# Kernel optimization log

Hardware: AMD Instinct MI355X
Metric: run time of the kernel (lower is better)

## Reference

```python
import jax, jax.numpy as jnp
import numpy as np

S, P = 64, 32          # scenes, pedestrians per scene (uniform)
N = S * P              # total pedestrians = 2048
H, E = 64, 64          # h_dim, embedding_dim
D1, D2 = 512, 1024     # mlp_pre_pool hidden, bottleneck_dim
EPS = 1e-5             # torch BatchNorm1d eps


def _batchnorm(x, gamma, beta):
    # Training-mode BN with per-scene batch stats (matches the per-scene
    # loop in the original, where BN sees one scene's num_ped^2 rows).
    # x: [S, P*P, D]
    mu = jnp.mean(x, axis=1, keepdims=True)
    var = jnp.mean(jnp.square(x - mu), axis=1, keepdims=True)  # biased var, as torch BN
    return (x - mu) * jax.lax.rsqrt(var + EPS) * gamma + beta


def setup_inputs() -> dict:
    key = jax.random.key(0)
    ks = jax.random.split(key, 16)
    h_states = jax.random.normal(ks[0], (1, N, H), jnp.float32)
    starts = jnp.arange(S, dtype=jnp.int32) * P
    seq_start_end = jnp.stack([starts, starts + P], axis=1)  # [S, 2]
    end_pos = jax.random.normal(ks[1], (N, 2), jnp.float32)
    rel_pos = jax.random.normal(ks[2], (N, 2), jnp.float32)  # unused (pooling_dim=2) but a fwd arg
    sc = 0.05
    params = dict(
        W_embed=jax.random.normal(ks[3], (2, E), jnp.float32) * sc,
        b_embed=jnp.zeros((E,), jnp.float32),
        W1=jax.random.normal(ks[4], (E + H, D1), jnp.float32) * sc,
        b1=jnp.zeros((D1,), jnp.float32),
        g1=jnp.ones((D1,), jnp.float32),
        be1=jnp.zeros((D1,), jnp.float32),
        W2=jax.random.normal(ks[5], (D1, D2), jnp.float32) * sc,
        b2=jnp.zeros((D2,), jnp.float32),
        g2=jnp.ones((D2,), jnp.float32),
        be2=jnp.zeros((D2,), jnp.float32),
    )
    return dict(h_states=h_states, seq_start_end=seq_start_end,
                end_pos=end_pos, rel_pos=rel_pos, **params)


def reference(h_states, seq_start_end, end_pos, rel_pos,
              W_embed, b_embed, W1, b1, g1, be1, W2, b2, g2, be2):
    # Uniform scenes: seq_start_end delimits S contiguous blocks of P peds.
    pos = end_pos.reshape(S, P, 2)
    h = h_states.reshape(N, H).reshape(S, P, H)
    # Original indexing: row (k*P + j) -> pos[j] - pos[k], hidden[j];
    # the final view(P, P, -1).max(1) maxes over j for each k.
    rel = pos[:, None, :, :] - pos[:, :, None, :]          # [S, Pk, Pj, 2]
    emb = rel @ W_embed + b_embed                          # [S, Pk, Pj, E]
    hid = jnp.broadcast_to(h[:, None, :, :], (S, P, P, H)) # hidden of j
    x = jnp.concatenate([emb, hid], axis=-1).reshape(S, P * P, E + H)
    x = jax.nn.relu(_batchnorm(x @ W1 + b1, g1, be1))      # [S, P*P, 512]
    x = jax.nn.relu(_batchnorm(x @ W2 + b2, g2, be2))      # [S, P*P, 1024]
    pool_h = x.reshape(S, P, P, D2).max(axis=2)            # max over j
    return pool_h.reshape(N, D2)
```

## Files before the change

### kernel.cpp

```cpp
#include <hip/hip_runtime.h>
#include <hip/hip_bf16.h>

#define S_ 64
#define P_ 32
#define N_ 2048
#define H_ 64
#define E_ 64
#define D1_ 512
#define D2_ 1024
#define EPS_ 1e-5f

typedef unsigned short u16;
using bf16x8 = __attribute__((ext_vector_type(8))) __bf16;
using floatx4 = __attribute__((ext_vector_type(4))) float;

__device__ inline u16 f2bf(float x) {
    unsigned u = __float_as_uint(x);
    unsigned r = (u + 0x7fffu + ((u >> 16) & 1u)) >> 16;
    return (u16)r;
}
__device__ inline unsigned bf2pack(float lo, float hi) {
    return (unsigned)f2bf(lo) | ((unsigned)f2bf(hi) << 16);
}

__global__ __launch_bounds__(512)
void k_prep(const float* __restrict__ pos, const float* __restrict__ h,
            const float* __restrict__ We, const float* __restrict__ W1,
            const float* __restrict__ g1, const float* __restrict__ be1,
            const float* __restrict__ W2,
            float* __restrict__ A, float* __restrict__ Bv, u16* __restrict__ w2t) {
    __shared__ float smem[64 * 65];
    const int bid = blockIdx.x;
    const int tid = threadIdx.x;
    if (bid < S_) {
        const int s = bid;
        const int d = tid;
        float* hs = smem;
        float* ps = smem + 2048;
        for (int i = tid; i < P_ * H_; i += 512) hs[i] = h[(size_t)s * P_ * H_ + i];
        if (tid < 64) ps[tid] = pos[s * 64 + tid];
        __syncthreads();
        float wq0 = 0.f, wq1 = 0.f;
        for (int e = 0; e < E_; ++e) {
            float wv = W1[e * D1_ + d];
            wq0 += We[e] * wv;
            wq1 += We[E_ + e] * wv;
        }
        float w[P_];
#pragma unroll
        for (int j = 0; j < P_; ++j) w[j] = 0.f;
        const float4* h4 = (const float4*)hs;
        for (int e4 = 0; e4 < 16; ++e4) {
            const float c0 = W1[(E_ + e4 * 4 + 0) * D1_ + d];
            const float c1 = W1[(E_ + e4 * 4 + 1) * D1_ + d];
            const float c2 = W1[(E_ + e4 * 4 + 2) * D1_ + d];
            const float c3 = W1[(E_ + e4 * 4 + 3) * D1_ + d];
#pragma unroll
            for (int j = 0; j < P_; ++j) {
                float4 hv = h4[j * 16 + e4];
                w[j] += hv.x * c0 + hv.y * c1 + hv.z * c2 + hv.w * c3;
            }
        }
        float sw = 0.f, sww = 0.f, su = 0.f, suu = 0.f;
#pragma unroll
        for (int j = 0; j < P_; ++j) {
            float u = ps[2 * j] * wq0 + ps[2 * j + 1] * wq1;
            w[j] += u;
            sw += w[j]; sww += w[j] * w[j];
            su += u;    suu += u * u;
        }
        const float mw = sw * (1.f / P_), mu = su * (1.f / P_);
        const float var = (sww * (1.f / P_) - mw * mw) + (suu * (1.f / P_) - mu * mu);
        const float sc = rsqrtf(var + EPS_) * g1[d];
        const float bb = be1[d];
#pragma unroll
        for (int j = 0; j < P_; ++j) {
            float u = ps[2 * j] * wq0 + ps[2 * j + 1] * wq1;
            A[(size_t)(s * P_ + j) * D1_ + d] = (w[j] - mw) * sc + bb;
            Bv[(size_t)(s * P_ + j) * D1_ + d] = (u - mu) * sc;
        }
    } else {
        const int b2 = bid - S_;
        const int bi = b2 & 15;
        const int bj = b2 >> 4;
        const int tx = tid & 63, ty = tid >> 6;
        float (*tile)[65] = (float (*)[65])smem;
#pragma unroll
        for (int i = 0; i < 64; i += 8)
            tile[ty + i][tx] = W2[(size_t)(bj * 64 + ty + i) * D2_ + bi * 64 + tx];
        __syncthreads();
#pragma unroll
        for (int i = 0; i < 64; i += 8)
            w2t[(size_t)(bi * 64 + ty + i) * D1_ + bj * 64 + tx] = f2bf(tile[tx][ty + i]);
    }
}

__global__ __launch_bounds__(256, 2)
void k_gemm(const float* __restrict__ A, const float* __restrict__ B,
            const u16* __restrict__ w2t,
            float* __restrict__ maxv, float* __restrict__ minv,
            float* __restrict__ psum, float* __restrict__ psumsq) {
    __shared__ u16 As[128 * 64];
    __shared__ u16 Ws[256 * 64];
    const int cs = blockIdx.x;
    const int mt = blockIdx.y;
    const int s = mt >> 3, rb = mt & 7;
    const int pedb = rb << 2;
    const int N0 = cs << 8;
    const int tid = threadIdx.x;
    const int wave = tid >> 6, lane = tid & 63;
    const int wm = wave >> 1, wn = wave & 1;
    const int quad = lane >> 4, l16 = lane & 15;
    const int lrow = lane >> 3, lchk = lane & 7;
    const int gchk = lchk ^ lrow;

    const int sj = tid >> 3, sc8 = tid & 7;
    const float* Aj = A + ((size_t)(s * 32 + sj) << 9) + (sc8 << 3);
    const float* Bp = B + ((size_t)(s * 32 + pedb) << 9) + (sc8 << 3);
    const int swz = (sc8 ^ (sj & 7)) << 3;

    floatx4 acc[4][8] = {};

    for (int it = 0; it < 8; ++it) {
        const int k0 = it << 6;
#pragma unroll
        for (int t = 0; t < 8; ++t) {
            const int rbase = (wave << 6) + (t << 3);
            const u16* gb = w2t + (size_t)(N0 + rbase + lrow) * D1_ + (k0 + (gchk << 3));
            __builtin_amdgcn_global_load_lds(
                (const __attribute__((address_space(1))) void*)gb,
                (__attribute__((address_space(3))) void*)(Ws + (rbase << 6)), 16, 0, 0);
        }
#pragma unroll
        for (int p = 0; p < 4; ++p) {
            const int r = (p << 5) + sj;
            const float4 alo = *(const float4*)(Aj + k0);
            const float4 ahi = *(const float4*)(Aj + k0 + 4);
            const float4 blo = *(const float4*)(Bp + ((size_t)p << 9) + k0);
            const float4 bhi = *(const float4*)(Bp + ((size_t)p << 9) + k0 + 4);
            uint4 o;
            o.x = bf2pack(fmaxf(alo.x - blo.x, 0.f), fmaxf(alo.y - blo.y, 0.f));
            o.y = bf2pack(fmaxf(alo.z - blo.z, 0.f), fmaxf(alo.w - blo.w, 0.f));
            o.z = bf2pack(fmaxf(ahi.x - bhi.x, 0.f), fmaxf(ahi.y - bhi.y, 0.f));
            o.w = bf2pack(fmaxf(ahi.z - bhi.z, 0.f), fmaxf(ahi.w - bhi.w, 0.f));
            *(uint4*)(As + (r << 6) + swz) = o;
        }
        __syncthreads();
#pragma unroll
        for (int kk = 0; kk < 2; ++kk) {
            const int ck = (kk << 2) + quad;
            const int po = (ck ^ (l16 & 7)) << 3;
            bf16x8 af[4], wf[8];
#pragma unroll
            for (int tm = 0; tm < 4; ++tm) {
                const int row = (wm << 6) + (tm << 4) + l16;
                af[tm] = *(const bf16x8*)(As + (row << 6) + po);
            }
#pragma unroll
            for (int tn = 0; tn < 8; ++tn) {
                const int row = (wn << 7) + (tn << 4) + l16;
                wf[tn] = *(const bf16x8*)(Ws + (row << 6) + po);
            }
#pragma unroll
            for (int tm = 0; tm < 4; ++tm)
#pragma unroll
                for (int tn = 0; tn < 8; ++tn)
                    acc[tm][tn] = __builtin_amdgcn_mfma_f32_16x16x32_bf16(
                        af[tm], wf[tn], acc[tm][tn], 0, 0, 0);
        }
        __syncthreads();
    }

#pragma unroll
    for (int tn = 0; tn < 8; ++tn) {
        const int col = N0 + (wn << 7) + (tn << 4) + l16;
        float wsum = 0.f, wsq = 0.f;
#pragma unroll
        for (int gp = 0; gp < 2; ++gp) {
            float vmax = -3.4e38f, vmin = 3.4e38f, vs = 0.f, vq = 0.f;
#pragma unroll
            for (int tm = gp * 2; tm < gp * 2 + 2; ++tm)
#pragma unroll
                for (int r = 0; r < 4; ++r) {
                    float v = acc[tm][tn][r];
                    vmax = fmaxf(vmax, v);
                    vmin = fminf(vmin, v);
                    vs += v;
                    vq += v * v;
                }
#pragma unroll
            for (int off = 16; off < 64; off <<= 1) {
                vmax = fmaxf(vmax, __shfl_xor(vmax, off));
                vmin = fminf(vmin, __shfl_xor(vmin, off));
                vs += __shfl_xor(vs, off);
                vq += __shfl_xor(vq, off);
            }
            if (quad == 0) {
                const int kg = s * 32 + pedb + (wm << 1) + gp;
                maxv[(size_t)kg * D2_ + col] = vmax;
                minv[(size_t)kg * D2_ + col] = vmin;
            }
            wsum += vs;
            wsq += vq;
        }
        if (quad == 0) {
            const int slot = (s << 4) + (rb << 1) + wm;
            psum[(size_t)slot * D2_ + col] = wsum;
            psumsq[(size_t)slot * D2_ + col] = wsq;
        }
    }
}

__global__ void k_final(const float* __restrict__ maxv, const float* __restrict__ minv,
                        const float* __restrict__ psum, const float* __restrict__ psumsq,
                        const float* __restrict__ g2, const float* __restrict__ be2,
                        float* __restrict__ out) {
    const int c = blockIdx.x * 256 + threadIdx.x;
    const int s = blockIdx.y;
    float sm = 0.f, sq = 0.f;
#pragma unroll
    for (int t = 0; t < 16; ++t) {
        sm += psum[(size_t)(s * 16 + t) * D2_ + c];
        sq += psumsq[(size_t)(s * 16 + t) * D2_ + c];
    }
    const float mu = sm * (1.f / 1024.f);
    const float var = sq * (1.f / 1024.f) - mu * mu;
    const float inv = rsqrtf(var + EPS_);
    const float scale = g2[c] * inv;
    const float bb = be2[c];
    const float* src = (scale >= 0.f) ? maxv : minv;
    for (int k = 0; k < 32; ++k) {
        const float v = src[(size_t)(s * 32 + k) * D2_ + c];
        out[(size_t)(s * 32 + k) * D2_ + c] = fmaxf((v - mu) * scale + bb, 0.f);
    }
}

extern "C" void kernel_launch(void* const* d_in, const int* in_sizes, int n_in,
                              void* d_out, int out_size, void* d_ws, size_t ws_size,
                              hipStream_t stream) {
    const float* h_states = (const float*)d_in[0];
    const float* end_pos = (const float*)d_in[2];
    const float* W_embed = (const float*)d_in[4];
    const float* W1 = (const float*)d_in[6];
    const float* g1 = (const float*)d_in[8];
    const float* be1 = (const float*)d_in[9];
    const float* W2 = (const float*)d_in[10];
    const float* g2 = (const float*)d_in[12];
    const float* be2 = (const float*)d_in[13];
    float* out = (float*)d_out;

    float* Abuf = (float*)d_ws;
    float* Bbuf = Abuf + 1048576;
    float* maxv = Bbuf + 1048576;
    float* minv = maxv + 2097152;
    float* psum = minv + 2097152;
    float* psumsq = psum + 1048576;
    u16* w2t = (u16*)(psumsq + 1048576);

    k_prep<<<dim3(S_ + 128), dim3(512), 0, stream>>>(end_pos, h_states, W_embed, W1,
                                                     g1, be1, W2, Abuf, Bbuf, w2t);
    k_gemm<<<dim3(4, 512), dim3(256), 0, stream>>>(Abuf, Bbuf, w2t, maxv, minv, psum, psumsq);
    k_final<<<dim3(4, 64), dim3(256), 0, stream>>>(maxv, minv, psum, psumsq, g2, be2, out);
}
```

Before: 199.1 us.

## Split prep across d-quarters and widen GEMM tile to 512 columns with 8 waves

The prep kernel now uses 256 blocks instead of 64, each covering a quarter of the D1 dimension with four pedestrian groups. Per-column BN statistics are combined through a shared-memory reduction, which gives more parallelism and fewer registers per thread. The GEMM kernel moves to 512-thread blocks covering 512 output columns, so each A tile (built with relu(A-B) and bf16 conversion) is reused across twice as many columns and the grid is halved. The trade-off is a doubled W2 tile in LDS and the launch bound of 512 threads with 4 blocks, which may cause register or occupancy pressure.

```diff
diff --git a/kernel.cpp b/kernel.cpp
--- a/kernel.cpp
+++ b/kernel.cpp
@@ -29,26 +29,28 @@
             const float* __restrict__ g1, const float* __restrict__ be1,
             const float* __restrict__ W2,
             float* __restrict__ A, float* __restrict__ Bv, u16* __restrict__ w2t) {
-    __shared__ float smem[64 * 65];
+    __shared__ float smem[4160];
     const int bid = blockIdx.x;
     const int tid = threadIdx.x;
-    if (bid < S_) {
-        const int s = bid;
-        const int d = tid;
+    if (bid < 256) {
+        const int s = bid >> 2, dq = bid & 3;
+        const int jg = tid >> 7, dl = tid & 127;
+        const int d = (dq << 7) + dl;
         float* hs = smem;
         float* ps = smem + 2048;
+        float* red = smem + 2112;
         for (int i = tid; i < P_ * H_; i += 512) hs[i] = h[(size_t)s * P_ * H_ + i];
         if (tid < 64) ps[tid] = pos[s * 64 + tid];
         __syncthreads();
         float wq0 = 0.f, wq1 = 0.f;
         for (int e = 0; e < E_; ++e) {
-            float wv = W1[e * D1_ + d];
+            const float wv = W1[e * D1_ + d];
             wq0 += We[e] * wv;
             wq1 += We[E_ + e] * wv;
         }
-        float w[P_];
-#pragma unroll
-        for (int j = 0; j < P_; ++j) w[j] = 0.f;
+        float w[8], u[8];
+#pragma unroll
+        for (int jj = 0; jj < 8; ++jj) w[jj] = 0.f;
         const float4* h4 = (const float4*)hs;
         for (int e4 = 0; e4 < 16; ++e4) {
             const float c0 = W1[(E_ + e4 * 4 + 0) * D1_ + d];
@@ -56,31 +58,45 @@
             const float c2 = W1[(E_ + e4 * 4 + 2) * D1_ + d];
             const float c3 = W1[(E_ + e4 * 4 + 3) * D1_ + d];
 #pragma unroll
-            for (int j = 0; j < P_; ++j) {
-                float4 hv = h4[j * 16 + e4];
-                w[j] += hv.x * c0 + hv.y * c1 + hv.z * c2 + hv.w * c3;
+            for (int jj = 0; jj < 8; ++jj) {
+                const float4 hv = h4[((jg << 3) + jj) * 16 + e4];
+                w[jj] += hv.x * c0 + hv.y * c1 + hv.z * c2 + hv.w * c3;
             }
         }
         float sw = 0.f, sww = 0.f, su = 0.f, suu = 0.f;
 #pragma unroll
-        for (int j = 0; j < P_; ++j) {
-            float u = ps[2 * j] * wq0 + ps[2 * j + 1] * wq1;
-            w[j] += u;
-            sw += w[j]; sww += w[j] * w[j];
-            su += u;    suu += u * u;
-        }
-        const float mw = sw * (1.f / P_), mu = su * (1.f / P_);
-        const float var = (sww * (1.f / P_) - mw * mw) + (suu * (1.f / P_) - mu * mu);
+        for (int jj = 0; jj < 8; ++jj) {
+            const int j = (jg << 3) + jj;
+            u[jj] = ps[2 * j] * wq0 + ps[2 * j + 1] * wq1;
+            w[jj] += u[jj];
+            sw += w[jj]; sww += w[jj] * w[jj];
+            su += u[jj]; suu += u[jj] * u[jj];
+        }
+        red[(jg << 7) + dl] = sw;
+        red[512 + (jg << 7) + dl] = sww;
+        red[1024 + (jg << 7) + dl] = su;
+        red[1536 + (jg << 7) + dl] = suu;
+        __syncthreads();
+        float tw = 0.f, tww = 0.f, tu = 0.f, tuu = 0.f;
+#pragma unroll
+        for (int g = 0; g < 4; ++g) {
+            tw += red[(g << 7) + dl];
+            tww += red[512 + (g << 7) + dl];
+            tu += red[1024 + (g << 7) + dl];
+            tuu += red[1536 + (g << 7) + dl];
+        }
+        const float mw = tw * (1.f / P_), mu = tu * (1.f / P_);
+        const float var = (tww * (1.f / P_) - mw * mw) + (tuu * (1.f / P_) - mu * mu);
         const float sc = rsqrtf(var + EPS_) * g1[d];
         const float bb = be1[d];
 #pragma unroll
-        for (int j = 0; j < P_; ++j) {
-            float u = ps[2 * j] * wq0 + ps[2 * j + 1] * wq1;
-            A[(size_t)(s * P_ + j) * D1_ + d] = (w[j] - mw) * sc + bb;
-            Bv[(size_t)(s * P_ + j) * D1_ + d] = (u - mu) * sc;
+        for (int jj = 0; jj < 8; ++jj) {
+            const int j = (jg << 3) + jj;
+            A[(size_t)(s * P_ + j) * D1_ + d] = (w[jj] - mw) * sc + bb;
+            Bv[(size_t)(s * P_ + j) * D1_ + d] = (u[jj] - mu) * sc;
         }
     } else {
-        const int b2 = bid - S_;
+        const int b2 = bid - 256;
         const int bi = b2 & 15;
         const int bj = b2 >> 4;
         const int tx = tid & 63, ty = tid >> 6;
@@ -95,29 +111,24 @@
     }
 }
 
-__global__ __launch_bounds__(256, 2)
+__global__ __launch_bounds__(512, 4)
 void k_gemm(const float* __restrict__ A, const float* __restrict__ B,
             const u16* __restrict__ w2t,
             float* __restrict__ maxv, float* __restrict__ minv,
             float* __restrict__ psum, float* __restrict__ psumsq) {
     __shared__ u16 As[128 * 64];
-    __shared__ u16 Ws[256 * 64];
+    __shared__ u16 Ws[512 * 64];
     const int cs = blockIdx.x;
     const int mt = blockIdx.y;
     const int s = mt >> 3, rb = mt & 7;
     const int pedb = rb << 2;
-    const int N0 = cs << 8;
+    const int N0 = cs << 9;
     const int tid = threadIdx.x;
     const int wave = tid >> 6, lane = tid & 63;
-    const int wm = wave >> 1, wn = wave & 1;
+    const int wm = wave >> 2, wn = wave & 3;
     const int quad = lane >> 4, l16 = lane & 15;
     const int lrow = lane >> 3, lchk = lane & 7;
     const int gchk = lchk ^ lrow;
-
-    const int sj = tid >> 3, sc8 = tid & 7;
-    const float* Aj = A + ((size_t)(s * 32 + sj) << 9) + (sc8 << 3);
-    const float* Bp = B + ((size_t)(s * 32 + pedb) << 9) + (sc8 << 3);
-    const int swz = (sc8 ^ (sj & 7)) << 3;
 
     floatx4 acc[4][8] = {};
 
@@ -132,18 +143,22 @@
                 (__attribute__((address_space(3))) void*)(Ws + (rbase << 6)), 16, 0, 0);
         }
 #pragma unroll
-        for (int p = 0; p < 4; ++p) {
-            const int r = (p << 5) + sj;
-            const float4 alo = *(const float4*)(Aj + k0);
-            const float4 ahi = *(const float4*)(Aj + k0 + 4);
-            const float4 blo = *(const float4*)(Bp + ((size_t)p << 9) + k0);
-            const float4 bhi = *(const float4*)(Bp + ((size_t)p << 9) + k0 + 4);
+        for (int t = 0; t < 2; ++t) {
+            const int slot = tid + (t << 9);
+            const int r = slot >> 3, c = slot & 7;
+            const int j = r & 31, p = r >> 5;
+            const float* Aj = A + ((size_t)(s * 32 + j) << 9) + (c << 3) + k0;
+            const float* Bp = B + ((size_t)(s * 32 + pedb + p) << 9) + (c << 3) + k0;
+            const float4 alo = *(const float4*)Aj;
+            const float4 ahi = *(const float4*)(Aj + 4);
+            const float4 blo = *(const float4*)Bp;
+            const float4 bhi = *(const float4*)(Bp + 4);
             uint4 o;
             o.x = bf2pack(fmaxf(alo.x - blo.x, 0.f), fmaxf(alo.y - blo.y, 0.f));
             o.y = bf2pack(fmaxf(alo.z - blo.z, 0.f), fmaxf(alo.w - blo.w, 0.f));
             o.z = bf2pack(fmaxf(ahi.x - bhi.x, 0.f), fmaxf(ahi.y - bhi.y, 0.f));
             o.w = bf2pack(fmaxf(ahi.z - bhi.z, 0.f), fmaxf(ahi.w - bhi.w, 0.f));
-            *(uint4*)(As + (r << 6) + swz) = o;
+            *(uint4*)(As + (r << 6) + ((c ^ (r & 7)) << 3)) = o;
         }
         __syncthreads();
 #pragma unroll
@@ -182,7 +197,7 @@
             for (int tm = gp * 2; tm < gp * 2 + 2; ++tm)
 #pragma unroll
                 for (int r = 0; r < 4; ++r) {
-                    float v = acc[tm][tn][r];
+                    const float v = acc[tm][tn][r];
                     vmax = fmaxf(vmax, v);
                     vmin = fminf(vmin, v);
                     vs += v;
@@ -257,8 +272,8 @@
     float* psumsq = psum + 1048576;
     u16* w2t = (u16*)(psumsq + 1048576);
 
-    k_prep<<<dim3(S_ + 128), dim3(512), 0, stream>>>(end_pos, h_states, W_embed, W1,
-                                                     g1, be1, W2, Abuf, Bbuf, w2t);
-    k_gemm<<<dim3(4, 512), dim3(256), 0, stream>>>(Abuf, Bbuf, w2t, maxv, minv, psum, psumsq);
+    k_prep<<<dim3(384), dim3(512), 0, stream>>>(end_pos, h_states, W_embed, W1,
+                                                g1, be1, W2, Abuf, Bbuf, w2t);
+    k_gemm<<<dim3(2, 512), dim3(512), 0, stream>>>(Abuf, Bbuf, w2t, maxv, minv, psum, psumsq);
     k_final<<<dim3(4, 64), dim3(256), 0, stream>>>(maxv, minv, psum, psumsq, g2, be2, out);
 }
```

Result: slower. 684.6 us (+243.9%).

## Fuse prep, GEMM and finalize into one cooperative persistent kernel

Applied to the files above, without the earlier changes.

Merges the three launches into a single cooperative kernel that uses grid-wide syncs between the prep, GEMM and finalize phases. Each GEMM block now owns one M-tile and loops over all four column slices, where previously each block handled one (column slice, M-tile) pair. Prep is split into 256-thread units covering a quarter of the D1 columns, with a shared-memory reduction for the BN1 statistics. The aim is to remove launch gaps and kernel-boundary drains. The cost is fewer concurrent blocks and serialized column slices inside each block, which may reduce parallelism in the GEMM phase. A fallback path with three separate launches is kept.

```diff
diff --git a/kernel.cpp b/kernel.cpp
--- a/kernel.cpp
+++ b/kernel.cpp
@@ -1,5 +1,8 @@
 #include <hip/hip_runtime.h>
 #include <hip/hip_bf16.h>
+#include <hip/hip_cooperative_groups.h>
+
+namespace cg = cooperative_groups;
 
 #define S_ 64
 #define P_ 32
@@ -23,205 +26,208 @@
     return (unsigned)f2bf(lo) | ((unsigned)f2bf(hi) << 16);
 }
 
-__global__ __launch_bounds__(512)
-void k_prep(const float* __restrict__ pos, const float* __restrict__ h,
-            const float* __restrict__ We, const float* __restrict__ W1,
-            const float* __restrict__ g1, const float* __restrict__ be1,
-            const float* __restrict__ W2,
-            float* __restrict__ A, float* __restrict__ Bv, u16* __restrict__ w2t) {
-    __shared__ float smem[64 * 65];
-    const int bid = blockIdx.x;
-    const int tid = threadIdx.x;
-    if (bid < S_) {
-        const int s = bid;
-        const int d = tid;
-        float* hs = smem;
-        float* ps = smem + 2048;
-        for (int i = tid; i < P_ * H_; i += 512) hs[i] = h[(size_t)s * P_ * H_ + i];
-        if (tid < 64) ps[tid] = pos[s * 64 + tid];
-        __syncthreads();
-        float wq0 = 0.f, wq1 = 0.f;
-        for (int e = 0; e < E_; ++e) {
-            float wv = W1[e * D1_ + d];
-            wq0 += We[e] * wv;
-            wq1 += We[E_ + e] * wv;
+
+__device__ void prep_scene_256(int u, int tid, float* smem,
+                               const float* __restrict__ pos, const float* __restrict__ h,
+                               const float* __restrict__ We, const float* __restrict__ W1,
+                               const float* __restrict__ g1, const float* __restrict__ be1,
+                               float* __restrict__ A, float* __restrict__ Bv) {
+    const int s = u >> 2, dq = u & 3;
+    const int jg = tid >> 7, dl = tid & 127;
+    const int d = (dq << 7) + dl;
+    float* hs = smem;
+    float* ps = smem + 2048;
+    float* red = smem + 2112;
+    for (int i = tid; i < 2048; i += 256) hs[i] = h[(size_t)s * 2048 + i];
+    if (tid < 64) ps[tid] = pos[s * 64 + tid];
+    __syncthreads();
+    float wq0 = 0.f, wq1 = 0.f;
+    for (int e = 0; e < 64; ++e) {
+        const float wv = W1[e * 512 + d];
+        wq0 += We[e] * wv;
+        wq1 += We[64 + e] * wv;
+    }
+    float w[16], uu[16];
+#pragma unroll
+    for (int jj = 0; jj < 16; ++jj) w[jj] = 0.f;
+    const float4* h4 = (const float4*)hs;
+    for (int e4 = 0; e4 < 16; ++e4) {
+        const float c0 = W1[(64 + e4 * 4 + 0) * 512 + d];
+        const float c1 = W1[(64 + e4 * 4 + 1) * 512 + d];
+        const float c2 = W1[(64 + e4 * 4 + 2) * 512 + d];
+        const float c3 = W1[(64 + e4 * 4 + 3) * 512 + d];
+#pragma unroll
+        for (int jj = 0; jj < 16; ++jj) {
+            const float4 hv = h4[((jg << 4) + jj) * 16 + e4];
+            w[jj] += hv.x * c0 + hv.y * c1 + hv.z * c2 + hv.w * c3;
         }
-        float w[P_];
-#pragma unroll
-        for (int j = 0; j < P_; ++j) w[j] = 0.f;
-        const float4* h4 = (const float4*)hs;
-        for (int e4 = 0; e4 < 16; ++e4) {
-            const float c0 = W1[(E_ + e4 * 4 + 0) * D1_ + d];
-            const float c1 = W1[(E_ + e4 * 4 + 1) * D1_ + d];
-            const float c2 = W1[(E_ + e4 * 4 + 2) * D1_ + d];
-            const float c3 = W1[(E_ + e4 * 4 + 3) * D1_ + d];
-#pragma unroll
-            for (int j = 0; j < P_; ++j) {
-                float4 hv = h4[j * 16 + e4];
-                w[j] += hv.x * c0 + hv.y * c1 + hv.z * c2 + hv.w * c3;
-            }
-        }
-        float sw = 0.f, sww = 0.f, su = 0.f, suu = 0.f;
-#pragma unroll
-        for (int j = 0; j < P_; ++j) {
-            float u = ps[2 * j] * wq0 + ps[2 * j + 1] * wq1;
-            w[j] += u;
-            sw += w[j]; sww += w[j] * w[j];
-            su += u;    suu += u * u;
-        }
-        const float mw = sw * (1.f / P_), mu = su * (1.f / P_);
-        const float var = (sww * (1.f / P_) - mw * mw) + (suu * (1.f / P_) - mu * mu);
-        const float sc = rsqrtf(var + EPS_) * g1[d];
-        const float bb = be1[d];
-#pragma unroll
-        for (int j = 0; j < P_; ++j) {
-            float u = ps[2 * j] * wq0 + ps[2 * j + 1] * wq1;
-            A[(size_t)(s * P_ + j) * D1_ + d] = (w[j] - mw) * sc + bb;
-            Bv[(size_t)(s * P_ + j) * D1_ + d] = (u - mu) * sc;
-        }
-    } else {
-        const int b2 = bid - S_;
-        const int bi = b2 & 15;
-        const int bj = b2 >> 4;
-        const int tx = tid & 63, ty = tid >> 6;
-        float (*tile)[65] = (float (*)[65])smem;
-#pragma unroll
-        for (int i = 0; i < 64; i += 8)
-            tile[ty + i][tx] = W2[(size_t)(bj * 64 + ty + i) * D2_ + bi * 64 + tx];
-        __syncthreads();
-#pragma unroll
-        for (int i = 0; i < 64; i += 8)
-            w2t[(size_t)(bi * 64 + ty + i) * D1_ + bj * 64 + tx] = f2bf(tile[tx][ty + i]);
-    }
-}
-
-__global__ __launch_bounds__(256, 2)
-void k_gemm(const float* __restrict__ A, const float* __restrict__ B,
-            const u16* __restrict__ w2t,
-            float* __restrict__ maxv, float* __restrict__ minv,
-            float* __restrict__ psum, float* __restrict__ psumsq) {
-    __shared__ u16 As[128 * 64];
-    __shared__ u16 Ws[256 * 64];
-    const int cs = blockIdx.x;
-    const int mt = blockIdx.y;
-    const int s = mt >> 3, rb = mt & 7;
-    const int pedb = rb << 2;
-    const int N0 = cs << 8;
-    const int tid = threadIdx.x;
+    }
+    float sw = 0.f, sww = 0.f, su = 0.f, suu = 0.f;
+#pragma unroll
+    for (int jj = 0; jj < 16; ++jj) {
+        const int j = (jg << 4) + jj;
+        uu[jj] = ps[2 * j] * wq0 + ps[2 * j + 1] * wq1;
+        w[jj] += uu[jj];
+        sw += w[jj]; sww += w[jj] * w[jj];
+        su += uu[jj]; suu += uu[jj] * uu[jj];
+    }
+    red[(jg << 7) + dl] = sw;
+    red[256 + (jg << 7) + dl] = sww;
+    red[512 + (jg << 7) + dl] = su;
+    red[768 + (jg << 7) + dl] = suu;
+    __syncthreads();
+    const float tw = red[dl] + red[128 + dl];
+    const float tww = red[256 + dl] + red[384 + dl];
+    const float tu = red[512 + dl] + red[640 + dl];
+    const float tuu = red[768 + dl] + red[896 + dl];
+    const float mw = tw * (1.f / 32.f), mu2 = tu * (1.f / 32.f);
+    const float var = (tww * (1.f / 32.f) - mw * mw) + (tuu * (1.f / 32.f) - mu2 * mu2);
+    const float sc = rsqrtf(var + EPS_) * g1[d];
+    const float bb = be1[d];
+#pragma unroll
+    for (int jj = 0; jj < 16; ++jj) {
+        const int j = (jg << 4) + jj;
+        A[(size_t)(s * 32 + j) * 512 + d] = (w[jj] - mw) * sc + bb;
+        Bv[(size_t)(s * 32 + j) * 512 + d] = (uu[jj] - mu2) * sc;
+    }
+}
+
+__device__ void w2t_tile_256(int b2, int tid, void* smem,
+                             const float* __restrict__ W2, u16* __restrict__ w2t) {
+    float (*tile)[65] = (float (*)[65])smem;
+    const int bi = b2 & 15, bj = b2 >> 4;
+    const int tx = tid & 63, ty = tid >> 6;
+#pragma unroll
+    for (int i = 0; i < 64; i += 4)
+        tile[ty + i][tx] = W2[(size_t)(bj * 64 + ty + i) * 1024 + bi * 64 + tx];
+    __syncthreads();
+#pragma unroll
+    for (int i = 0; i < 64; i += 4)
+        w2t[(size_t)(bi * 64 + ty + i) * 512 + bj * 64 + tx] = f2bf(tile[tx][ty + i]);
+}
+
+__device__ void gemm_mtile(int mt, int tid, u16* As, u16* Ws,
+                           const float* __restrict__ A, const float* __restrict__ Bv,
+                           const u16* __restrict__ w2t,
+                           float* __restrict__ maxv, float* __restrict__ minv,
+                           float* __restrict__ psum, float* __restrict__ psumsq) {
     const int wave = tid >> 6, lane = tid & 63;
     const int wm = wave >> 1, wn = wave & 1;
     const int quad = lane >> 4, l16 = lane & 15;
     const int lrow = lane >> 3, lchk = lane & 7;
     const int gchk = lchk ^ lrow;
-
     const int sj = tid >> 3, sc8 = tid & 7;
-    const float* Aj = A + ((size_t)(s * 32 + sj) << 9) + (sc8 << 3);
-    const float* Bp = B + ((size_t)(s * 32 + pedb) << 9) + (sc8 << 3);
+    const int s2 = mt >> 3, rb = mt & 7;
+    const int pedb = rb << 2;
+    const float* Aj = A + ((size_t)(s2 * 32 + sj) << 9) + (sc8 << 3);
+    const float* Bp = Bv + ((size_t)(s2 * 32 + pedb) << 9) + (sc8 << 3);
     const int swz = (sc8 ^ (sj & 7)) << 3;
 
-    floatx4 acc[4][8] = {};
-
-    for (int it = 0; it < 8; ++it) {
-        const int k0 = it << 6;
-#pragma unroll
-        for (int t = 0; t < 8; ++t) {
-            const int rbase = (wave << 6) + (t << 3);
-            const u16* gb = w2t + (size_t)(N0 + rbase + lrow) * D1_ + (k0 + (gchk << 3));
-            __builtin_amdgcn_global_load_lds(
-                (const __attribute__((address_space(1))) void*)gb,
-                (__attribute__((address_space(3))) void*)(Ws + (rbase << 6)), 16, 0, 0);
+    for (int cs = 0; cs < 4; ++cs) {
+        const int N0 = cs << 8;
+        floatx4 acc[4][8] = {};
+        for (int it = 0; it < 8; ++it) {
+            const int k0 = it << 6;
+#pragma unroll
+            for (int t = 0; t < 8; ++t) {
+                const int rbase = (wave << 6) + (t << 3);
+                const u16* gb = w2t + (size_t)(N0 + rbase + lrow) * 512 + (k0 + (gchk << 3));
+                __builtin_amdgcn_global_load_lds(
+                    (const __attribute__((address_space(1))) void*)gb,
+                    (__attribute__((address_space(3))) void*)(Ws + (rbase << 6)), 16, 0, 0);
+            }
+#pragma unroll
+            for (int p = 0; p < 4; ++p) {
+                const int r = (p << 5) + sj;
+                const float4 alo = *(const float4*)(Aj + k0);
+                const float4 ahi = *(const float4*)(Aj + k0 + 4);
+                const float4 blo = *(const float4*)(Bp + ((size_t)p << 9) + k0);
+                const float4 bhi = *(const float4*)(Bp + ((size_t)p << 9) + k0 + 4);
+                uint4 o;
+                o.x = bf2pack(fmaxf(alo.x - blo.x, 0.f), fmaxf(alo.y - blo.y, 0.f));
+                o.y = bf2pack(fmaxf(alo.z - blo.z, 0.f), fmaxf(alo.w - blo.w, 0.f));
+                o.z = bf2pack(fmaxf(ahi.x - bhi.x, 0.f), fmaxf(ahi.y - bhi.y, 0.f));
+                o.w = bf2pack(fmaxf(ahi.z - bhi.z, 0.f), fmaxf(ahi.w - bhi.w, 0.f));
+                *(uint4*)(As + (r << 6) + swz) = o;
+            }
+            __syncthreads();
+#pragma unroll
+            for (int kk = 0; kk < 2; ++kk) {
+                const int ck = (kk << 2) + quad;
+                const int po = (ck ^ (l16 & 7)) << 3;
+                bf16x8 af[4], wf[8];
+#pragma unroll
+                for (int tm = 0; tm < 4; ++tm) {
+                    const int row = (wm << 6) + (tm << 4) + l16;
+                    af[tm] = *(const bf16x8*)(As + (row << 6) + po);
+                }
+#pragma unroll
+                for (int tn = 0; tn < 8; ++tn) {
+                    const int wrow = (wn << 7) + (tn << 4) + l16;
+                    wf[tn] = *(const bf16x8*)(Ws + (wrow << 6) + ((ck ^ (wrow & 7)) << 3));
+                }
+#pragma unroll
+                for (int tm = 0; tm < 4; ++tm)
+#pragma unroll
+                    for (int tn = 0; tn < 8; ++tn)
+                        acc[tm][tn] = __builtin_amdgcn_mfma_f32_16x16x32_bf16(
+                            af[tm], wf[tn], acc[tm][tn], 0, 0, 0);
+            }
+            __syncthreads();
         }
 #pragma unroll
-        for (int p = 0; p < 4; ++p) {
-            const int r = (p << 5) + sj;
-            const float4 alo = *(const float4*)(Aj + k0);
-            const float4 ahi = *(const float4*)(Aj + k0 + 4);
-            const float4 blo = *(const float4*)(Bp + ((size_t)p << 9) + k0);
-            const float4 bhi = *(const float4*)(Bp + ((size_t)p << 9) + k0 + 4);
-            uint4 o;
-            o.x = bf2pack(fmaxf(alo.x - blo.x, 0.f), fmaxf(alo.y - blo.y, 0.f));
-            o.y = bf2pack(fmaxf(alo.z - blo.z, 0.f), fmaxf(alo.w - blo.w, 0.f));
-            o.z = bf2pack(fmaxf(ahi.x - bhi.x, 0.f), fmaxf(ahi.y - bhi.y, 0.f));
-            o.w = bf2pack(fmaxf(ahi.z - bhi.z, 0.f), fmaxf(ahi.w - bhi.w, 0.f));
-            *(uint4*)(As + (r << 6) + swz) = o;
+        for (int tn = 0; tn < 8; ++tn) {
+            const int col = N0 + (wn << 7) + (tn << 4) + l16;
+            float wsum = 0.f, wsq = 0.f;
+#pragma unroll
+            for (int gp = 0; gp < 2; ++gp) {
+                float vmax = -3.4e38f, vmin = 3.4e38f, vs = 0.f, vq = 0.f;
+#pragma unroll
+                for (int tm = gp * 2; tm < gp * 2 + 2; ++tm)
+#pragma unroll
+                    for (int r = 0; r < 4; ++r) {
+                        const float v = acc[tm][tn][r];
+                        vmax = fmaxf(vmax, v);
+                        vmin = fminf(vmin, v);
+                        vs += v;
+                        vq += v * v;
+                    }
+#pragma unroll
+                for (int off = 16; off < 64; off <<= 1) {
+                    vmax = fmaxf(vmax, __shfl_xor(vmax, off));
+                    vmin = fminf(vmin, __shfl_xor(vmin, off));
+                    vs += __shfl_xor(vs, off);
+                    vq += __shfl_xor(vq, off);
+                }
+                if (quad == 0) {
+                    const int kg = s2 * 32 + pedb + (wm << 1) + gp;
+                    maxv[(size_t)kg * 1024 + col] = vmax;
+                    minv[(size_t)kg * 1024 + col] = vmin;
+                }
+                wsum += vs;
+                wsq += vq;
+            }
+            if (quad == 0) {
+                const int slot = (s2 << 4) + (rb << 1) + wm;
+                psum[(size_t)slot * 1024 + col] = wsum;
+                psumsq[(size_t)slot * 1024 + col] = wsq;
+            }
         }
-        __syncthreads();
-#pragma unroll
-        for (int kk = 0; kk < 2; ++kk) {
-            const int ck = (kk << 2) + quad;
-            const int po = (ck ^ (l16 & 7)) << 3;
-            bf16x8 af[4], wf[8];
-#pragma unroll
-            for (int tm = 0; tm < 4; ++tm) {
-                const int row = (wm << 6) + (tm << 4) + l16;
-                af[tm] = *(const bf16x8*)(As + (row << 6) + po);
-            }
-#pragma unroll
-            for (int tn = 0; tn < 8; ++tn) {
-                const int row = (wn << 7) + (tn << 4) + l16;
-                wf[tn] = *(const bf16x8*)(Ws + (row << 6) + po);
-            }
-#pragma unroll
-            for (int tm = 0; tm < 4; ++tm)
-#pragma unroll
-                for (int tn = 0; tn < 8; ++tn)
-                    acc[tm][tn] = __builtin_amdgcn_mfma_f32_16x16x32_bf16(
-                        af[tm], wf[tn], acc[tm][tn], 0, 0, 0);
-        }
-        __syncthreads();
-    }
-
-#pragma unroll
-    for (int tn = 0; tn < 8; ++tn) {
-        const int col = N0 + (wn << 7) + (tn << 4) + l16;
-        float wsum = 0.f, wsq = 0.f;
-#pragma unroll
-        for (int gp = 0; gp < 2; ++gp) {
-            float vmax = -3.4e38f, vmin = 3.4e38f, vs = 0.f, vq = 0.f;
-#pragma unroll
-            for (int tm = gp * 2; tm < gp * 2 + 2; ++tm)
-#pragma unroll
-                for (int r = 0; r < 4; ++r) {
-                    float v = acc[tm][tn][r];
-                    vmax = fmaxf(vmax, v);
-                    vmin = fminf(vmin, v);
-                    vs += v;
-                    vq += v * v;
-                }
-#pragma unroll
-            for (int off = 16; off < 64; off <<= 1) {
-                vmax = fmaxf(vmax, __shfl_xor(vmax, off));
-                vmin = fminf(vmin, __shfl_xor(vmin, off));
-                vs += __shfl_xor(vs, off);
-                vq += __shfl_xor(vq, off);
-            }
-            if (quad == 0) {
-                const int kg = s * 32 + pedb + (wm << 1) + gp;
-                maxv[(size_t)kg * D2_ + col] = vmax;
-                minv[(size_t)kg * D2_ + col] = vmin;
-            }
-            wsum += vs;
-            wsq += vq;
-        }
-        if (quad == 0) {
-            const int slot = (s << 4) + (rb << 1) + wm;
-            psum[(size_t)slot * D2_ + col] = wsum;
-            psumsq[(size_t)slot * D2_ + col] = wsq;
-        }
-    }
-}
-
-__global__ void k_final(const float* __restrict__ maxv, const float* __restrict__ minv,
-                        const float* __restrict__ psum, const float* __restrict__ psumsq,
-                        const float* __restrict__ g2, const float* __restrict__ be2,
-                        float* __restrict__ out) {
-    const int c = blockIdx.x * 256 + threadIdx.x;
-    const int s = blockIdx.y;
+    }
+}
+
+__device__ void final_unit_256(int u, int tid,
+                               const float* __restrict__ maxv, const float* __restrict__ minv,
+                               const float* __restrict__ psum, const float* __restrict__ psumsq,
+                               const float* __restrict__ g2, const float* __restrict__ be2,
+                               float* __restrict__ out) {
+    const int s3 = u >> 2;
+    const int c = ((u & 3) << 8) + tid;
     float sm = 0.f, sq = 0.f;
 #pragma unroll
     for (int t = 0; t < 16; ++t) {
-        sm += psum[(size_t)(s * 16 + t) * D2_ + c];
-        sq += psumsq[(size_t)(s * 16 + t) * D2_ + c];
+        sm += psum[(size_t)(s3 * 16 + t) * 1024 + c];
+        sq += psumsq[(size_t)(s3 * 16 + t) * 1024 + c];
     }
     const float mu = sm * (1.f / 1024.f);
     const float var = sq * (1.f / 1024.f) - mu * mu;
@@ -230,9 +236,79 @@
     const float bb = be2[c];
     const float* src = (scale >= 0.f) ? maxv : minv;
     for (int k = 0; k < 32; ++k) {
-        const float v = src[(size_t)(s * 32 + k) * D2_ + c];
-        out[(size_t)(s * 32 + k) * D2_ + c] = fmaxf((v - mu) * scale + bb, 0.f);
-    }
+        const float v = src[(size_t)(s3 * 32 + k) * 1024 + c];
+        out[(size_t)(s3 * 32 + k) * 1024 + c] = fmaxf((v - mu) * scale + bb, 0.f);
+    }
+}
+
+__global__ __launch_bounds__(256, 2)
+void k_all(const float* __restrict__ pos, const float* __restrict__ h,
+           const float* __restrict__ We, const float* __restrict__ W1,
+           const float* __restrict__ g1, const float* __restrict__ be1,
+           const float* __restrict__ W2, const float* __restrict__ g2,
+           const float* __restrict__ be2,
+           float* __restrict__ A, float* __restrict__ Bv, u16* __restrict__ w2t,
+           float* __restrict__ maxv, float* __restrict__ minv,
+           float* __restrict__ psum, float* __restrict__ psumsq,
+           float* __restrict__ out) {
+    __shared__ __align__(16) char smem_raw[49152];
+    cg::grid_group grid = cg::this_grid();
+    const int b = blockIdx.x;
+    const int g = gridDim.x;
+    const int tid = threadIdx.x;
+
+    for (int u = b; u < 384; u += g) {
+        if (u < 256)
+            prep_scene_256(u, tid, (float*)smem_raw, pos, h, We, W1, g1, be1, A, Bv);
+        else
+            w2t_tile_256(u - 256, tid, smem_raw, W2, w2t);
+        __syncthreads();
+    }
+    __threadfence();
+    grid.sync();
+
+    {
+        u16* As = (u16*)smem_raw;
+        u16* Ws = (u16*)(smem_raw + 16384);
+        for (int mt = b; mt < 512; mt += g)
+            gemm_mtile(mt, tid, As, Ws, A, Bv, w2t, maxv, minv, psum, psumsq);
+    }
+    __threadfence();
+    grid.sync();
+
+    for (int u = b; u < 256; u += g)
+        final_unit_256(u, tid, maxv, minv, psum, psumsq, g2, be2, out);
+}
+
+__global__ __launch_bounds__(256)
+void k_prep_fb(const float* __restrict__ pos, const float* __restrict__ h,
+               const float* __restrict__ We, const float* __restrict__ W1,
+               const float* __restrict__ g1, const float* __restrict__ be1,
+               const float* __restrict__ W2,
+               float* __restrict__ A, float* __restrict__ Bv, u16* __restrict__ w2t) {
+    __shared__ __align__(16) char smem_raw[16912];
+    const int bid = blockIdx.x;
+    if (bid < 256)
+        prep_scene_256(bid, threadIdx.x, (float*)smem_raw, pos, h, We, W1, g1, be1, A, Bv);
+    else
+        w2t_tile_256(bid - 256, threadIdx.x, smem_raw, W2, w2t);
+}
+
+__global__ __launch_bounds__(256, 2)
+void k_gemm_fb(const float* __restrict__ A, const float* __restrict__ Bv,
+               const u16* __restrict__ w2t,
+               float* __restrict__ maxv, float* __restrict__ minv,
+               float* __restrict__ psum, float* __restrict__ psumsq) {
+    __shared__ __align__(16) char smem_raw[49152];
+    gemm_mtile(blockIdx.x, threadIdx.x, (u16*)smem_raw, (u16*)(smem_raw + 16384),
+               A, Bv, w2t, maxv, minv, psum, psumsq);
+}
+
+__global__ void k_final_fb(const float* __restrict__ maxv, const float* __restrict__ minv,
+                           const float* __restrict__ psum, const float* __restrict__ psumsq,
+                           const float* __restrict__ g2, const float* __restrict__ be2,
+                           float* __restrict__ out) {
+    final_unit_256(blockIdx.x, threadIdx.x, maxv, minv, psum, psumsq, g2, be2, out);
 }
 
 extern "C" void kernel_launch(void* const* d_in, const int* in_sizes, int n_in,
@@ -257,8 +333,27 @@
     float* psumsq = psum + 1048576;
     u16* w2t = (u16*)(psumsq + 1048576);
 
-    k_prep<<<dim3(S_ + 128), dim3(512), 0, stream>>>(end_pos, h_states, W_embed, W1,
-                                                     g1, be1, W2, Abuf, Bbuf, w2t);
-    k_gemm<<<dim3(4, 512), dim3(256), 0, stream>>>(Abuf, Bbuf, w2t, maxv, minv, psum, psumsq);
-    k_final<<<dim3(4, 64), dim3(256), 0, stream>>>(maxv, minv, psum, psumsq, g2, be2, out);
-}
+    int coop_ok = 0, occ = 0, ncu = 0, dev = 0;
+    hipGetDevice(&dev);
+    hipDeviceGetAttribute(&coop_ok, hipDeviceAttributeCooperativeLaunch, dev);
+    hipDeviceGetAttribute(&ncu, hipDeviceAttributeMultiprocessorCount, dev);
+    hipOccupancyMaxActiveBlocksPerMultiprocessor(&occ, (const void*)k_all, 256, 0);
+    int grid = occ * ncu;
+    if (grid > 512) grid = 512;
+
+    if (coop_ok && grid >= 64) {
+        void* args[] = {
+            (void*)&end_pos, (void*)&h_states, (void*)&W_embed, (void*)&W1,
+            (void*)&g1, (void*)&be1, (void*)&W2, (void*)&g2, (void*)&be2,
+            (void*)&Abuf, (void*)&Bbuf, (void*)&w2t,
+            (void*)&maxv, (void*)&minv, (void*)&psum, (void*)&psumsq, (void*)&out
+        };
+        hipError_t e = hipLaunchCooperativeKernel((void*)k_all, dim3(grid), dim3(256),
+                                                  args, 0, stream);
+        if (e == hipSuccess) return;
+    }
+    k_prep_fb<<<dim3(384), dim3(256), 0, stream>>>(end_pos, h_states, W_embed, W1,
+                                                   g1, be1, W2, Abuf, Bbuf, w2t);
+    k_gemm_fb<<<dim3(512), dim3(256), 0, stream>>>(Abuf, Bbuf, w2t, maxv, minv, psum, psumsq);
+    k_final_fb<<<dim3(256), dim3(256), 0, stream>>>(maxv, minv, psum, psumsq, g2, be2, out);
+}
```

New measurement: 439.5 us. 121% more time.
